# Performance work log

Measured on AMD Instinct MI355X. Metric: run time of the kernel, lower is better.

Reference implementation:

```python
import jax, jax.numpy as jnp
import numpy as np

HID = 1152
NUM_HEADS = 16
NUM_MSK = 2
MLP_HID = int(HID * 4.0)
SCALE = (HID // NUM_HEADS) ** -0.5
EPS = 1e-6


def _ln(t):
    # LayerNorm, elementwise_affine=False, eps=1e-6
    mu = jnp.mean(t, axis=-1, keepdims=True)
    var = jnp.mean(jnp.square(t - mu), axis=-1, keepdims=True)
    return (t - mu) / jnp.sqrt(var + EPS)


def _modulate(t, shift, scale):
    return t * (1.0 + scale[:, None, :]) + shift[:, None, :]


def setup_inputs() -> dict:
    key = jax.random.key(0)
    ks = jax.random.split(key, 12)
    s = 0.02
    return {
        "x": jax.random.normal(ks[0], (8, 4096, HID), jnp.float32),
        "c": jax.random.normal(ks[1], (8, HID), jnp.float32),
        # adaLN_modulation_x: Linear(HID, 6*HID), stored as [in, out]
        "w_ada": jax.random.normal(ks[2], (HID, 6 * HID), jnp.float32) * s,
        "b_ada": jnp.zeros((6 * HID,), jnp.float32),
        # lin1: Linear(HID, 2*HID)
        "w1": jax.random.normal(ks[3], (HID, 2 * HID), jnp.float32) * s,
        "b1": jnp.zeros((2 * HID,), jnp.float32),
        # lin2: Linear(HID, HID)
        "w2": jax.random.normal(ks[4], (HID, HID), jnp.float32) * s,
        "b2": jnp.zeros((HID,), jnp.float32),
        # Mlp: fc1(HID->MLP_HID), gelu(tanh), fc2(MLP_HID->HID)
        "w_fc1": jax.random.normal(ks[5], (HID, MLP_HID), jnp.float32) * s,
        "b_fc1": jnp.zeros((MLP_HID,), jnp.float32),
        "w_fc2": jax.random.normal(ks[6], (MLP_HID, HID), jnp.float32) * s,
        "b_fc2": jnp.zeros((HID,), jnp.float32),
    }


def reference(x, c, w_ada, b_ada, w1, b1, w2, b2, w_fc1, b_fc1, w_fc2, b_fc2):
    B, N, C = x.shape
    # adaLN modulation: SiLU -> Linear, chunk 6 along feature dim
    mods = jax.nn.silu(c) @ w_ada + b_ada  # [B, 6C]
    sh_msa, sc_msa, g_msa, sh_mlp, sc_mlp, g_mlp = jnp.split(mods, 6, axis=1)

    # tiny key/value set from first num_msk tokens
    x0 = x[:, :NUM_MSK, :]  # [B, M, C]
    kv = _modulate(_ln(x0), sh_msa, sc_msa) @ w1 + b1  # [B, M, 2C]
    k, v = jnp.split(kv, 2, axis=2)  # each [B, M, C]
    q = _modulate(_ln(x), sh_msa, sc_msa) @ w2 + b2  # [B, N, C]

    attn = jax.nn.softmax(jnp.einsum("bnc,bmc->bnm", q, k) * SCALE, axis=-1)
    y = jnp.einsum("bnm,bmc->bnc", attn, v)  # [B, N, C]
    # faithful to torch: .transpose(1,2).reshape(B,N,C) (axis scramble, single head)
    y = jnp.swapaxes(y, 1, 2).reshape(B, N, C)
    y = y + g_msa[:, None, :] * y

    h = _modulate(_ln(y), sh_mlp, sc_mlp)
    mlp = jax.nn.gelu(h @ w_fc1 + b_fc1, approximate=True) @ w_fc2 + b_fc2
    return y + g_mlp[:, None, :] * mlp
```

## Files before the change

kernel.cpp:

```cpp
#include <hip/hip_runtime.h>
#include <hip/hip_bf16.h>

#define DEV __device__ __forceinline__

typedef unsigned short u16;
typedef short short8 __attribute__((ext_vector_type(8)));
typedef float f32x4 __attribute__((ext_vector_type(4)));
typedef unsigned long long ulv2 __attribute__((ext_vector_type(2)));

constexpr int HID  = 1152;
constexpr int NSEQ = 4096;
constexpr int NB   = 8;
constexpr int MROWS = NB * NSEQ;
constexpr int MLP  = 4608;
constexpr int NPAD2 = 1280;
constexpr float EPSV  = 1e-6f;
constexpr float SCALE = 0.11785113019775793f;

constexpr size_t O_WT1  = 0;
constexpr size_t SZ_WT1 = (size_t)MLP * HID * 2;
constexpr size_t O_WT2  = O_WT1 + SZ_WT1;
constexpr size_t SZ_WT2 = (size_t)NPAD2 * MLP * 2;
constexpr size_t O_H    = O_WT2 + SZ_WT2;
constexpr size_t SZ_H   = (size_t)MROWS * HID * 2;
constexpr size_t O_MODS = O_H + SZ_H;
constexpr size_t O_K    = O_MODS + (size_t)NB*6912*4;
constexpr size_t O_V    = O_K + (size_t)16*HID*4;
constexpr size_t O_U    = O_V + (size_t)16*HID*4;
constexpr size_t O_A1   = O_U + (size_t)16*HID*4;
constexpr size_t O_S0   = O_A1 + (size_t)16*HID*4;
constexpr size_t O_S1   = O_S0 + 64;
constexpr size_t O_P    = O_S1 + 64;
constexpr size_t O_ACT  = O_P + (size_t)NB*NSEQ*2*4;

#define BARR  asm volatile("s_barrier" ::: "memory")
#define VMW0  asm volatile("s_waitcnt vmcnt(0)" ::: "memory")
#define VMW4  asm volatile("s_waitcnt vmcnt(4)" ::: "memory")
#define VMW8  asm volatile("s_waitcnt vmcnt(8)" ::: "memory")
#define SP1   __builtin_amdgcn_s_setprio(1)
#define SP0   __builtin_amdgcn_s_setprio(0)

DEV u16 f2bf(float f){
  __hip_bfloat16 h = __float2bfloat16(f);
  u16 u; __builtin_memcpy(&u, &h, 2); return u;
}

DEV float wsum(float v){
  #pragma unroll
  for (int o = 32; o; o >>= 1) v += __shfl_xor(v, o, 64);
  return v;
}

DEV void cp16(void* lds, const void* g){
  __builtin_amdgcn_global_load_lds(
      (__attribute__((address_space(1))) void*)g,
      (__attribute__((address_space(3))) void*)lds, 16, 0, 0);
}

__global__ void tcast_k(const float* __restrict__ in, u16* __restrict__ out, int K, int N){
  __shared__ float tile[32][33];
  int n0 = blockIdx.x * 32, k0 = blockIdx.y * 32;
  int tx = threadIdx.x, ty = threadIdx.y;
  #pragma unroll
  for (int i = 0; i < 32; i += 8)
    tile[ty + i][tx] = in[(size_t)(k0 + ty + i) * N + (n0 + tx)];
  __syncthreads();
  #pragma unroll
  for (int i = 0; i < 32; i += 8)
    out[(size_t)(n0 + ty + i) * K + (k0 + tx)] = f2bf(tile[tx][ty + i]);
}

__global__ void mods_k(const float* __restrict__ cv, const float* __restrict__ w_ada,
                       const float* __restrict__ b_ada, float* __restrict__ modsb){
  int b = blockIdx.y;
  __shared__ float cs[HID];
  int tid = threadIdx.x;
  for (int i = tid; i < HID; i += 256){
    float t = cv[b*HID + i];
    cs[i] = t / (1.f + __expf(-t));
  }
  __syncthreads();
  int col = blockIdx.x * 256 + tid;
  float acc = b_ada[col];
  #pragma unroll 4
  for (int k = 0; k < HID; k++) acc += cs[k] * w_ada[(size_t)k*6912 + col];
  modsb[b*6912 + col] = acc;
}

__global__ void kv_k(const float* __restrict__ x, const float* __restrict__ modsb,
                     const float* __restrict__ w1, const float* __restrict__ b1,
                     float* __restrict__ kbuf, float* __restrict__ vbuf){
  int bt = blockIdx.y; int b = bt >> 1, t = bt & 1;
  int tid = threadIdx.x;
  __shared__ float mx[HID];
  __shared__ float rbuf[8];
  __shared__ float s_mu, s_rs;
  const float* xr = x + ((size_t)b*NSEQ + t) * HID;
  float sx = 0.f, sxx = 0.f;
  for (int i = tid; i < HID; i += 256){ float v = xr[i]; sx += v; sxx += v*v; }
  sx = wsum(sx); sxx = wsum(sxx);
  int wave = tid >> 6, lane = tid & 63;
  if (lane == 0){ rbuf[wave] = sx; rbuf[4+wave] = sxx; }
  __syncthreads();
  if (tid == 0){
    float a = rbuf[0]+rbuf[1]+rbuf[2]+rbuf[3];
    float bb = rbuf[4]+rbuf[5]+rbuf[6]+rbuf[7];
    float mu = a * (1.f/HID);
    float var = bb * (1.f/HID) - mu*mu;
    s_mu = mu; s_rs = rsqrtf(var + EPSV);
  }
  __syncthreads();
  float mu = s_mu, rs = s_rs;
  const float* md = modsb + b*6912;
  for (int i = tid; i < HID; i += 256)
    mx[i] = (xr[i]-mu)*rs*(1.f + md[HID+i]) + md[i];
  __syncthreads();
  int col = blockIdx.x * 256 + tid;
  float acc = b1[col];
  #pragma unroll 4
  for (int k = 0; k < HID; k++) acc += mx[k] * w1[(size_t)k*2304 + col];
  if (col < HID) kbuf[bt*HID + col] = acc;
  else           vbuf[bt*HID + col - HID] = acc;
}

__global__ void u2_k(const float* __restrict__ w2, const float* __restrict__ kbuf,
                     const float* __restrict__ modsb, float* __restrict__ ub,
                     float* __restrict__ A1b){
  int bm = blockIdx.y; int b = bm >> 1;
  int tid = threadIdx.x, wave = tid >> 6, lane = tid & 63;
  __shared__ float ks[HID];
  for (int i = tid; i < HID; i += 256) ks[i] = kbuf[bm*HID + i];
  __syncthreads();
  const float* md = modsb + b*6912;
  int j0 = blockIdx.x*16 + wave*4;
  #pragma unroll
  for (int jj = 0; jj < 4; jj++){
    int j = j0 + jj;
    const float* wr = w2 + (size_t)j*HID;
    float acc = 0.f;
    for (int i = lane; i < HID; i += 64) acc += wr[i] * ks[i];
    acc = wsum(acc);
    if (lane == 0){
      ub[bm*HID + j] = acc;
      A1b[bm*HID + j] = (1.f + md[HID + j]) * acc;
    }
  }
}

__global__ void sred_k(const float* __restrict__ ub, const float* __restrict__ A1b,
                       const float* __restrict__ modsb, const float* __restrict__ b2,
                       const float* __restrict__ kbuf, float* __restrict__ S0,
                       float* __restrict__ S1){
  int bm = blockIdx.x; int b = bm >> 1;
  int tid = threadIdx.x;
  float s0 = 0.f, s1 = 0.f;
  const float* md = modsb + b*6912;
  for (int i = tid; i < HID; i += 256){
    s1 += A1b[bm*HID + i];
    s0 += md[i]*ub[bm*HID + i] + b2[i]*kbuf[bm*HID + i];
  }
  s0 = wsum(s0); s1 = wsum(s1);
  __shared__ float rb[16];
  int wave = tid >> 6, lane = tid & 63;
  if (lane == 0){ rb[wave] = s0; rb[8+wave] = s1; }
  __syncthreads();
  if (tid == 0){
    S0[bm] = rb[0]+rb[1]+rb[2]+rb[3];
    S1[bm] = rb[8]+rb[9]+rb[10]+rb[11];
  }
}

__global__ void p_k(const float* __restrict__ x, const float* __restrict__ A1b,
                    const float* __restrict__ S0, const float* __restrict__ S1,
                    float2* __restrict__ pb){
  int tid = threadIdx.x, wave = tid >> 6, lane = tid & 63;
  int row0 = blockIdx.x * 4;
  int b = row0 >> 12;
  __shared__ float a1s[2*HID];
  for (int i = tid; i < 2*HID; i += 256) a1s[i] = A1b[b*2*HID + i];
  __syncthreads();
  int row = row0 + wave;
  const float* xr = x + (size_t)row * HID;
  float sx = 0.f, sxx = 0.f, d0 = 0.f, d1 = 0.f;
  #pragma unroll
  for (int i = 0; i < 9; i++){
    int cc = lane*2 + i*128;
    float2 v = *(const float2*)(xr + cc);
    sx += v.x + v.y; sxx += v.x*v.x + v.y*v.y;
    d0 += v.x*a1s[cc]       + v.y*a1s[cc+1];
    d1 += v.x*a1s[HID+cc]   + v.y*a1s[HID+cc+1];
  }
  sx = wsum(sx); sxx = wsum(sxx); d0 = wsum(d0); d1 = wsum(d1);
  if (lane == 0){
    float mu = sx * (1.f/HID);
    float var = sxx * (1.f/HID) - mu*mu;
    float rs = rsqrtf(var + EPSV);
    float sc0 = rs*(d0 - mu*S1[b*2+0]) + S0[b*2+0];
    float sc1 = rs*(d1 - mu*S1[b*2+1]) + S0[b*2+1];
    float z = (sc0 - sc1) * SCALE;
    float p0 = 1.f / (1.f + __expf(-z));
    pb[row] = make_float2(p0, 1.f - p0);
  }
}

__global__ void h_k(const float2* __restrict__ pb, const float* __restrict__ vbuf,
                    const float* __restrict__ modsb, u16* __restrict__ H){
  int tid = threadIdx.x, wave = tid >> 6, lane = tid & 63;
  int row0 = blockIdx.x * 4;
  int b = row0 >> 12;
  __shared__ float gs[HID], shs[HID], scs[HID];
  const float* md = modsb + b*6912;
  for (int i = tid; i < HID; i += 256){
    gs[i]  = 1.f + md[2*HID + i];
    shs[i] = md[3*HID + i];
    scs[i] = 1.f + md[4*HID + i];
  }
  __syncthreads();
  int row = row0 + wave;
  int n = row & (NSEQ-1);
  const float2* pbb = pb + ((size_t)b << 12);
  const float* vb0 = vbuf + b*2*HID;
  float yv[18];
  float sx = 0.f, sxx = 0.f;
  #pragma unroll
  for (int i = 0; i < 9; i++){
    int cc = lane*2 + i*128;
    int f = n*HID + cc;
    int r0 = f & (NSEQ-1), ci0 = f >> 12;
    int f1 = f + 1;
    int r1 = f1 & (NSEQ-1), ci1 = f1 >> 12;
    float2 pv0 = pbb[r0];
    float2 pv1 = pbb[r1];
    float y0 = gs[cc]   * (pv0.x*vb0[ci0] + pv0.y*vb0[HID+ci0]);
    float y1 = gs[cc+1] * (pv1.x*vb0[ci1] + pv1.y*vb0[HID+ci1]);
    yv[2*i] = y0; yv[2*i+1] = y1;
    sx += y0 + y1; sxx += y0*y0 + y1*y1;
  }
  sx = wsum(sx); sxx = wsum(sxx);
  float mu = sx * (1.f/HID);
  float var = sxx * (1.f/HID) - mu*mu;
  float rs = rsqrtf(var + EPSV);
  u16* Hr = H + (size_t)row * HID;
  #pragma unroll
  for (int i = 0; i < 9; i++){
    int cc = lane*2 + i*128;
    ushort2 st;
    st.x = f2bf((yv[2*i]   - mu)*rs*scs[cc]   + shs[cc]);
    st.y = f2bf((yv[2*i+1] - mu)*rs*scs[cc+1] + shs[cc+1]);
    *(ushort2*)(Hr + cc) = st;
  }
}

template<int EPI, int KC>
__global__ __launch_bounds__(512, 2) void gemm8_k(
    const u16* __restrict__ A, const u16* __restrict__ Bt,
    int nTn,
    const float* __restrict__ bias,
    u16* __restrict__ outB, float* __restrict__ outF,
    const float2* __restrict__ p, const float* __restrict__ vbuf,
    const float* __restrict__ modsb, int rowOffset)
{
  __shared__ u16 lds[2][2][256*64];
  const int tid = threadIdx.x;
  const int wave = tid >> 6, lane = tid & 63;
  const int wm = wave >> 2, wn = wave & 3;

  int nwg = gridDim.x;
  int bid = blockIdx.x;
  int q = nwg >> 3;
  int w = (bid & 7) * q + (bid >> 3);
  int bm = w / nTn, bn = w - bm * nTn;

  const u16* Ab = A + (size_t)bm * 256 * KC;
  const u16* Bb = Bt + (size_t)bn * 256 * KC;

  f32x4 acc[8][4] = {};

  auto stage = [&](int buf, int ab, int half, int t){
    const u16* src = ab ? Bb : Ab;
    char* ldsb = (char*)&lds[buf][ab][0] + half*16384 + wave*2048 + lane*16;
    int rbase = half*128 + wave*16 + (lane>>3);
    int kof = t*64 + (((lane&7) ^ (lane>>3)) << 3);
    cp16(ldsb,        src + (size_t)rbase*KC + kof);
    cp16(ldsb + 1024, src + (size_t)(rbase+8)*KC + kof);
  };
  auto ldA = [&](short8 (&v)[4][2], int buf, int mh){
    const char* base = (const char*)&lds[buf][0][0];
    int colb = (((lane>>4)<<4)) ^ ((lane&7)<<4);
    #pragma unroll
    for (int f = 0; f < 4; f++){
      const char* rp = base + (wm*128 + mh*64 + f*16 + (lane&15))*128;
      v[f][0] = *(const short8*)(rp + colb);
      v[f][1] = *(const short8*)(rp + (colb ^ 64));
    }
  };
  auto ldB = [&](short8 (&v)[2][2], int buf, int nh){
    const char* base = (const char*)&lds[buf][1][0];
    int colb = (((lane>>4)<<4)) ^ ((lane&7)<<4);
    #pragma unroll
    for (int f = 0; f < 2; f++){
      const char* rp = base + (wn*64 + nh*32 + f*16 + (lane&15))*128;
      v[f][0] = *(const short8*)(rp + colb);
      v[f][1] = *(const short8*)(rp + (colb ^ 64));
    }
  };
  auto mm = [&](short8 (&a)[4][2], short8 (&b)[2][2], int mh, int nh){
    #pragma unroll
    for (int ks = 0; ks < 2; ks++)
      #pragma unroll
      for (int f = 0; f < 4; f++)
        #pragma unroll
        for (int g = 0; g < 2; g++)
          acc[mh*4+f][nh*2+g] = __builtin_amdgcn_mfma_f32_16x16x32_bf16(
              a[f][ks], b[g][ks], acc[mh*4+f][nh*2+g], 0, 0, 0);
  };

  short8 av[4][2], av2[4][2], bv[2][2], bv2[2][2];

  stage(0,0,0,0); stage(0,0,1,0); stage(0,1,0,0); stage(0,1,1,0);
  stage(1,1,0,1); stage(1,1,1,1); stage(1,0,0,1); stage(1,0,1,1);
  VMW8; BARR;

  constexpr int NIT = KC >> 7;
  for (int it = 0; it < NIT; ++it){
    const int t2 = 2*it + 2, t3 = 2*it + 3;
    const bool fin = (it == NIT-1);
    ldA(av, 0, 0); ldB(bv, 0, 0);
    SP1; mm(av, bv, 0, 0); SP0; BARR;
    ldB(bv2, 0, 1);
    SP1; mm(av, bv2, 0, 1); SP0; BARR;
    ldA(av2, 0, 1);
    if (!fin) stage(0,1,0,t2);
    SP1; mm(av2, bv, 1, 0); SP0; BARR;
    if (!fin){ stage(0,1,1,t2); VMW4; } else { VMW0; }
    SP1; mm(av2, bv2, 1, 1); SP0; BARR;
    ldA(av, 1, 0); ldB(bv, 1, 0);
    if (!fin){ stage(0,0,0,t2); stage(0,0,1,t2); }
    SP1; mm(av, bv, 0, 0); SP0; BARR;
    ldB(bv2, 1, 1);
    SP1; mm(av, bv2, 0, 1); SP0; BARR;
    ldA(av2, 1, 1);
    if (!fin) stage(1,1,0,t3);
    SP1; mm(av2, bv, 1, 0); SP0; BARR;
    if (!fin){ stage(1,1,1,t3); stage(1,0,0,t3); stage(1,0,1,t3); VMW8; }
    SP1; mm(av2, bv2, 1, 1); SP0; BARR;
  }

  int colBase = bn*256 + wn*64;
  int rowB = bm*256 + wm*128 + ((lane>>4)<<2);
  if constexpr (EPI == 0){
    u16* cs = (u16*)&lds[0][0][0];
    #pragma unroll
    for (int n = 0; n < 4; n++){
      int colL = wn*64 + n*16 + (lane&15);
      float bs = bias[bn*256 + colL];
      #pragma unroll
      for (int m = 0; m < 8; m++){
        #pragma unroll
        for (int r = 0; r < 4; r++){
          int rowL = wm*128 + m*16 + ((lane>>4)<<2) + r;
          float xv = acc[m][n][r] + bs;
          float t = xv * (1.f + 0.044715f * xv * xv);
          float g = xv / (1.f + __expf(-1.5957691216057308f * t));
          int bo = ((rowL*256 + colL)*2) ^ (((rowL>>2)&3)<<5);
          *(u16*)((char*)cs + bo) = f2bf(g);
        }
      }
    }
    __syncthreads();
    #pragma unroll
    for (int e = 0; e < 16; e++){
      int idx = e*512 + tid;
      int rowL = idx >> 5, c16 = idx & 31;
      int bo = (rowL*512 + c16*16) ^ (((rowL>>2)&3)<<5);
      ulv2 v = *(const ulv2*)((const char*)cs + bo);
      __builtin_nontemporal_store(v,
          (ulv2*)&outB[(size_t)(bm*256 + rowL)*MLP + bn*256 + c16*8]);
    }
  } else {
    int bIdx = (rowOffset + bm*256) >> 12;
    const float* md = modsb + bIdx*6912;
    const float2* pbb = p + ((size_t)bIdx << 12);
    const float* vb0 = vbuf + bIdx*2*HID;
    #pragma unroll
    for (int n = 0; n < 4; n++){
      int col = colBase + n*16 + (lane&15);
      if (col < HID){
        float bs = bias[col];
        float gmsa = 1.f + md[2*HID + col];
        float gmlp = md[5*HID + col];
        #pragma unroll
        for (int m = 0; m < 8; m++){
          #pragma unroll
          for (int r = 0; r < 4; r++){
            int grow = rowOffset + rowB + m*16 + r;
            int nn = grow & (NSEQ-1);
            int f = nn*HID + col;
            int rr = f & (NSEQ-1), ci = f >> 12;
            float2 pv = pbb[rr];
            float y2 = gmsa * (pv.x*vb0[ci] + pv.y*vb0[HID + ci]);
            __builtin_nontemporal_store(y2 + gmlp * (acc[m][n][r] + bs),
                &outF[(size_t)grow*HID + col]);
          }
        }
      }
    }
  }
}

extern "C" void kernel_launch(void* const* d_in, const int* in_sizes, int n_in,
                              void* d_out, int out_size, void* d_ws, size_t ws_size,
                              hipStream_t stream){
  const float* x     = (const float*)d_in[0];
  const float* cvec  = (const float*)d_in[1];
  const float* w_ada = (const float*)d_in[2];
  const float* b_ada = (const float*)d_in[3];
  const float* w1    = (const float*)d_in[4];
  const float* b1    = (const float*)d_in[5];
  const float* w2    = (const float*)d_in[6];
  const float* b2    = (const float*)d_in[7];
  const float* w_fc1 = (const float*)d_in[8];
  const float* b_fc1 = (const float*)d_in[9];
  const float* w_fc2 = (const float*)d_in[10];
  const float* b_fc2 = (const float*)d_in[11];
  float* out = (float*)d_out;
  char* ws = (char*)d_ws;

  u16*   Wt1   = (u16*)  (ws + O_WT1);
  u16*   Wt2   = (u16*)  (ws + O_WT2);
  u16*   Hb    = (u16*)  (ws + O_H);
  float* modsb = (float*)(ws + O_MODS);
  float* kb    = (float*)(ws + O_K);
  float* vb    = (float*)(ws + O_V);
  float* ub    = (float*)(ws + O_U);
  float* A1b   = (float*)(ws + O_A1);
  float* S0b   = (float*)(ws + O_S0);
  float* S1b   = (float*)(ws + O_S1);
  float2* pb   = (float2*)(ws + O_P);
  u16*   actb  = (u16*)  (ws + O_ACT);

  (void)hipMemsetAsync(ws + O_WT2 + (size_t)HID*MLP*2, 0, (size_t)(NPAD2-HID)*MLP*2, stream);

  tcast_k<<<dim3(MLP/32, HID/32), dim3(32,8), 0, stream>>>(w_fc1, Wt1, HID, MLP);
  tcast_k<<<dim3(HID/32, MLP/32), dim3(32,8), 0, stream>>>(w_fc2, Wt2, MLP, HID);
  mods_k<<<dim3(27, NB), 256, 0, stream>>>(cvec, w_ada, b_ada, modsb);
  kv_k<<<dim3(9, 16), 256, 0, stream>>>(x, modsb, w1, b1, kb, vb);
  u2_k<<<dim3(HID/16, 16), 256, 0, stream>>>(w2, kb, modsb, ub, A1b);
  sred_k<<<16, 256, 0, stream>>>(ub, A1b, modsb, b2, kb, S0b, S1b);
  p_k<<<MROWS/4, 256, 0, stream>>>(x, A1b, S0b, S1b, pb);
  h_k<<<MROWS/4, 256, 0, stream>>>(pb, vb, modsb, Hb);

  size_t actFull = (size_t)MROWS * MLP * 2;
  int nch = 1;
  while (nch < 8 && O_ACT + actFull/nch > ws_size) nch <<= 1;
  int rowsPer = MROWS / nch;

  for (int chn = 0; chn < nch; chn++){
    int r0 = chn * rowsPer;
    int nTm = rowsPer / 256;
    gemm8_k<0, HID><<<nTm*(MLP/256), 512, 0, stream>>>(
        Hb + (size_t)r0*HID, Wt1, MLP/256, b_fc1,
        actb, nullptr, nullptr, nullptr, nullptr, 0);
    gemm8_k<1, MLP><<<nTm*(NPAD2/256), 512, 0, stream>>>(
        actb, Wt2, NPAD2/256, b_fc2,
        nullptr, out, pb, vb, modsb, r0);
  }
  (void)in_sizes; (void)n_in; (void)out_size;
}
```

Baseline: 1.120 ms.

## Make GEMMs persistent and prefetch next tile during epilogue

Both MLP GEMMs now launch a fixed 256-workgroup persistent grid that loops over output tiles. The first K-slab of the next tile is prefetched into LDS during the last iteration, and the second slab is issued after the epilogue. The intent is to hide the pipeline fill and epilogue latency between tiles. The epilogues are restaged through the other LDS buffer in row passes, and the fc2 output now goes out as coalesced 16-byte stores instead of scattered scalar stores. This adds extra barriers, and the hand-counted vmcnt waits (24/40) must match the outstanding loads exactly.

Result: slower. 2.105 ms (+88.0%).

```diff
diff --git a/kernel.cpp b/kernel.cpp
--- a/kernel.cpp
+++ b/kernel.cpp
@@ -33,10 +33,12 @@
 constexpr size_t O_P    = O_S1 + 64;
 constexpr size_t O_ACT  = O_P + (size_t)NB*NSEQ*2*4;
 
-#define BARR  asm volatile("s_barrier" ::: "memory")
-#define VMW0  asm volatile("s_waitcnt vmcnt(0)" ::: "memory")
-#define VMW4  asm volatile("s_waitcnt vmcnt(4)" ::: "memory")
-#define VMW8  asm volatile("s_waitcnt vmcnt(8)" ::: "memory")
+#define BARR   asm volatile("s_barrier" ::: "memory")
+#define VMW0   asm volatile("s_waitcnt vmcnt(0)" ::: "memory")
+#define VMW4   asm volatile("s_waitcnt vmcnt(4)" ::: "memory")
+#define VMW8   asm volatile("s_waitcnt vmcnt(8)" ::: "memory")
+#define VMW24  asm volatile("s_waitcnt vmcnt(24)" ::: "memory")
+#define VMW40  asm volatile("s_waitcnt vmcnt(40)" ::: "memory")
 #define SP1   __builtin_amdgcn_s_setprio(1)
 #define SP0   __builtin_amdgcn_s_setprio(0)
 
@@ -252,9 +254,9 @@
 }
 
 template<int EPI, int KC>
-__global__ __launch_bounds__(512, 2) void gemm8_k(
+__global__ __launch_bounds__(512, 2) void gemmp_k(
     const u16* __restrict__ A, const u16* __restrict__ Bt,
-    int nTn,
+    int nTiles, int nTn,
     const float* __restrict__ bias,
     u16* __restrict__ outB, float* __restrict__ outF,
     const float2* __restrict__ p, const float* __restrict__ vbuf,
@@ -264,29 +266,22 @@
   const int tid = threadIdx.x;
   const int wave = tid >> 6, lane = tid & 63;
   const int wm = wave >> 2, wn = wave & 3;
-
-  int nwg = gridDim.x;
-  int bid = blockIdx.x;
-  int q = nwg >> 3;
-  int w = (bid & 7) * q + (bid >> 3);
-  int bm = w / nTn, bn = w - bm * nTn;
-
-  const u16* Ab = A + (size_t)bm * 256 * KC;
-  const u16* Bb = Bt + (size_t)bn * 256 * KC;
-
-  f32x4 acc[8][4] = {};
-
-  auto stage = [&](int buf, int ab, int half, int t){
-    const u16* src = ab ? Bb : Ab;
+  const int q = nTiles >> 3;
+
+  auto swz = [&](int bid, int& bm, int& bn){
+    int w = (bid & 7) * q + (bid >> 3);
+    bm = w / nTn; bn = w - bm * nTn;
+  };
+  auto stageTo = [&](int buf, int ab, int half, const u16* src, int tof){
     char* ldsb = (char*)&lds[buf][ab][0] + half*16384 + wave*2048 + lane*16;
     int rbase = half*128 + wave*16 + (lane>>3);
-    int kof = t*64 + (((lane&7) ^ (lane>>3)) << 3);
+    int kof = tof + (((lane&7) ^ (lane>>3)) << 3);
     cp16(ldsb,        src + (size_t)rbase*KC + kof);
     cp16(ldsb + 1024, src + (size_t)(rbase+8)*KC + kof);
   };
+  const int colb = (((lane>>4)<<4)) ^ ((lane&7)<<4);
   auto ldA = [&](short8 (&v)[4][2], int buf, int mh){
     const char* base = (const char*)&lds[buf][0][0];
-    int colb = (((lane>>4)<<4)) ^ ((lane&7)<<4);
     #pragma unroll
     for (int f = 0; f < 4; f++){
       const char* rp = base + (wm*128 + mh*64 + f*16 + (lane&15))*128;
@@ -296,7 +291,6 @@
   };
   auto ldB = [&](short8 (&v)[2][2], int buf, int nh){
     const char* base = (const char*)&lds[buf][1][0];
-    int colb = (((lane>>4)<<4)) ^ ((lane&7)<<4);
     #pragma unroll
     for (int f = 0; f < 2; f++){
       const char* rp = base + (wn*64 + nh*32 + f*16 + (lane&15))*128;
@@ -304,106 +298,163 @@
       v[f][1] = *(const short8*)(rp + (colb ^ 64));
     }
   };
-  auto mm = [&](short8 (&a)[4][2], short8 (&b)[2][2], int mh, int nh){
-    #pragma unroll
-    for (int ks = 0; ks < 2; ks++)
+
+  for (int tt = 0;; ++tt){
+    int bid = tid*0 + blockIdx.x + (int)gridDim.x * tt;
+    if (bid >= nTiles) break;
+    int bm, bn; swz(bid, bm, bn);
+    const u16* Ab = A + (size_t)bm * 256 * KC;
+    const u16* Bb = Bt + (size_t)bn * 256 * KC;
+    int bidN = bid + (int)gridDim.x;
+    const bool hasNext = bidN < nTiles;
+    int bmN = bm, bnN = bn;
+    if (hasNext) swz(bidN, bmN, bnN);
+    const u16* AbN = A + (size_t)bmN * 256 * KC;
+    const u16* BbN = Bt + (size_t)bnN * 256 * KC;
+
+    if (tt == 0){
+      stageTo(0,0,0,Ab,0);  stageTo(0,0,1,Ab,0);  stageTo(0,1,0,Bb,0);  stageTo(0,1,1,Bb,0);
+      stageTo(1,1,0,Bb,64); stageTo(1,1,1,Bb,64); stageTo(1,0,0,Ab,64); stageTo(1,0,1,Ab,64);
+      VMW8;
+    } else {
+      if constexpr (EPI == 0) { VMW24; } else { VMW40; }
+    }
+    BARR;
+
+    f32x4 acc[8][4] = {};
+    short8 av[4][2], av2[4][2], bv[2][2], bv2[2][2];
+    auto mm = [&](short8 (&a)[4][2], short8 (&b)[2][2], int mh, int nh){
       #pragma unroll
-      for (int f = 0; f < 4; f++)
+      for (int ks = 0; ks < 2; ks++)
         #pragma unroll
-        for (int g = 0; g < 2; g++)
-          acc[mh*4+f][nh*2+g] = __builtin_amdgcn_mfma_f32_16x16x32_bf16(
-              a[f][ks], b[g][ks], acc[mh*4+f][nh*2+g], 0, 0, 0);
-  };
-
-  short8 av[4][2], av2[4][2], bv[2][2], bv2[2][2];
-
-  stage(0,0,0,0); stage(0,0,1,0); stage(0,1,0,0); stage(0,1,1,0);
-  stage(1,1,0,1); stage(1,1,1,1); stage(1,0,0,1); stage(1,0,1,1);
-  VMW8; BARR;
-
-  constexpr int NIT = KC >> 7;
-  for (int it = 0; it < NIT; ++it){
-    const int t2 = 2*it + 2, t3 = 2*it + 3;
-    const bool fin = (it == NIT-1);
-    ldA(av, 0, 0); ldB(bv, 0, 0);
-    SP1; mm(av, bv, 0, 0); SP0; BARR;
-    ldB(bv2, 0, 1);
-    SP1; mm(av, bv2, 0, 1); SP0; BARR;
-    ldA(av2, 0, 1);
-    if (!fin) stage(0,1,0,t2);
-    SP1; mm(av2, bv, 1, 0); SP0; BARR;
-    if (!fin){ stage(0,1,1,t2); VMW4; } else { VMW0; }
-    SP1; mm(av2, bv2, 1, 1); SP0; BARR;
-    ldA(av, 1, 0); ldB(bv, 1, 0);
-    if (!fin){ stage(0,0,0,t2); stage(0,0,1,t2); }
-    SP1; mm(av, bv, 0, 0); SP0; BARR;
-    ldB(bv2, 1, 1);
-    SP1; mm(av, bv2, 0, 1); SP0; BARR;
-    ldA(av2, 1, 1);
-    if (!fin) stage(1,1,0,t3);
-    SP1; mm(av2, bv, 1, 0); SP0; BARR;
-    if (!fin){ stage(1,1,1,t3); stage(1,0,0,t3); stage(1,0,1,t3); VMW8; }
-    SP1; mm(av2, bv2, 1, 1); SP0; BARR;
-  }
-
-  int colBase = bn*256 + wn*64;
-  int rowB = bm*256 + wm*128 + ((lane>>4)<<2);
-  if constexpr (EPI == 0){
-    u16* cs = (u16*)&lds[0][0][0];
-    #pragma unroll
-    for (int n = 0; n < 4; n++){
-      int colL = wn*64 + n*16 + (lane&15);
-      float bs = bias[bn*256 + colL];
+        for (int f = 0; f < 4; f++)
+          #pragma unroll
+          for (int g = 0; g < 2; g++)
+            acc[mh*4+f][nh*2+g] = __builtin_amdgcn_mfma_f32_16x16x32_bf16(
+                a[f][ks], b[g][ks], acc[mh*4+f][nh*2+g], 0, 0, 0);
+    };
+
+    constexpr int NIT = KC >> 7;
+    for (int it = 0; it < NIT; ++it){
+      const bool fin = (it == NIT-1);
+      const u16* As2 = fin ? AbN : Ab;
+      const u16* Bs2 = fin ? BbN : Bb;
+      const int t2o = fin ? 0 : (2*it+2)*64;
+      const int t3o = (2*it+3)*64;
+      const bool do2 = !fin || hasNext;
+      ldA(av, 0, 0); ldB(bv, 0, 0);
+      SP1; mm(av, bv, 0, 0); SP0; BARR;
+      ldB(bv2, 0, 1);
+      SP1; mm(av, bv2, 0, 1); SP0; BARR;
+      ldA(av2, 0, 1);
+      if (do2) stageTo(0,1,0,Bs2,t2o);
+      SP1; mm(av2, bv, 1, 0); SP0; BARR;
+      if (do2){ stageTo(0,1,1,Bs2,t2o); VMW4; } else { VMW0; }
+      SP1; mm(av2, bv2, 1, 1); SP0; BARR;
+      ldA(av, 1, 0); ldB(bv, 1, 0);
+      if (do2){ stageTo(0,0,0,As2,t2o); stageTo(0,0,1,As2,t2o); }
+      SP1; mm(av, bv, 0, 0); SP0; BARR;
+      ldB(bv2, 1, 1);
+      SP1; mm(av, bv2, 0, 1); SP0; BARR;
+      ldA(av2, 1, 1);
+      if (!fin) stageTo(1,1,0,Bb,t3o);
+      SP1; mm(av2, bv, 1, 0); SP0; BARR;
+      if (!fin){ stageTo(1,1,1,Bb,t3o); stageTo(1,0,0,Ab,t3o); stageTo(1,0,1,Ab,t3o); VMW8; }
+      SP1; mm(av2, bv2, 1, 1); SP0; BARR;
+    }
+
+    if constexpr (EPI == 0){
+      u16* cs = (u16*)&lds[1][0][0];
       #pragma unroll
-      for (int m = 0; m < 8; m++){
-        #pragma unroll
-        for (int r = 0; r < 4; r++){
-          int rowL = wm*128 + m*16 + ((lane>>4)<<2) + r;
-          float xv = acc[m][n][r] + bs;
-          float t = xv * (1.f + 0.044715f * xv * xv);
-          float g = xv / (1.f + __expf(-1.5957691216057308f * t));
-          int bo = ((rowL*256 + colL)*2) ^ (((rowL>>2)&3)<<5);
-          *(u16*)((char*)cs + bo) = f2bf(g);
-        }
-      }
-    }
-    __syncthreads();
-    #pragma unroll
-    for (int e = 0; e < 16; e++){
-      int idx = e*512 + tid;
-      int rowL = idx >> 5, c16 = idx & 31;
-      int bo = (rowL*512 + c16*16) ^ (((rowL>>2)&3)<<5);
-      ulv2 v = *(const ulv2*)((const char*)cs + bo);
-      __builtin_nontemporal_store(v,
-          (ulv2*)&outB[(size_t)(bm*256 + rowL)*MLP + bn*256 + c16*8]);
-    }
-  } else {
-    int bIdx = (rowOffset + bm*256) >> 12;
-    const float* md = modsb + bIdx*6912;
-    const float2* pbb = p + ((size_t)bIdx << 12);
-    const float* vb0 = vbuf + bIdx*2*HID;
-    #pragma unroll
-    for (int n = 0; n < 4; n++){
-      int col = colBase + n*16 + (lane&15);
-      if (col < HID){
-        float bs = bias[col];
-        float gmsa = 1.f + md[2*HID + col];
-        float gmlp = md[5*HID + col];
-        #pragma unroll
-        for (int m = 0; m < 8; m++){
+      for (int pass = 0; pass < 2; ++pass){
+        if (wm == pass){
           #pragma unroll
-          for (int r = 0; r < 4; r++){
-            int grow = rowOffset + rowB + m*16 + r;
-            int nn = grow & (NSEQ-1);
-            int f = nn*HID + col;
-            int rr = f & (NSEQ-1), ci = f >> 12;
-            float2 pv = pbb[rr];
-            float y2 = gmsa * (pv.x*vb0[ci] + pv.y*vb0[HID + ci]);
-            __builtin_nontemporal_store(y2 + gmlp * (acc[m][n][r] + bs),
-                &outF[(size_t)grow*HID + col]);
+          for (int n = 0; n < 4; n++){
+            int colL = wn*64 + n*16 + (lane&15);
+            float bs = bias[bn*256 + colL];
+            #pragma unroll
+            for (int m = 0; m < 8; m++){
+              #pragma unroll
+              for (int r = 0; r < 4; r++){
+                int rowS = m*16 + ((lane>>4)<<2) + r;
+                float xv = acc[m][n][r] + bs;
+                float t = xv * (1.f + 0.044715f * xv * xv);
+                float g = xv / (1.f + __expf(-1.5957691216057308f * t));
+                int bo = ((rowS*256 + colL)*2) ^ (((rowS>>2)&3)<<5);
+                *(u16*)((char*)cs + bo) = f2bf(g);
+              }
+            }
           }
         }
+        __syncthreads();
+        #pragma unroll
+        for (int e = 0; e < 8; e++){
+          int idx = e*512 + tid;
+          int rowS = idx >> 5, c16 = idx & 31;
+          int bo = (rowS*512 + c16*16) ^ (((rowS>>2)&3)<<5);
+          ulv2 v = *(const ulv2*)((const char*)cs + bo);
+          __builtin_nontemporal_store(v,
+              (ulv2*)&outB[(size_t)(bm*256 + pass*128 + rowS)*MLP + bn*256 + c16*8]);
+        }
+        __syncthreads();
       }
+    } else {
+      float* cf = (float*)&lds[1][0][0];
+      int bIdx = (rowOffset + bm*256) >> 12;
+      const float* md = modsb + bIdx*6912;
+      const float2* pbb = p + ((size_t)bIdx << 12);
+      const float* vb0 = vbuf + bIdx*2*HID;
+      #pragma unroll
+      for (int pass = 0; pass < 4; ++pass){
+        if (wm == (pass>>1)){
+          int mb = (pass&1)*4;
+          #pragma unroll
+          for (int n = 0; n < 4; n++){
+            int colL = wn*64 + n*16 + (lane&15);
+            int col = bn*256 + colL;
+            float bs = 0.f, gmsa = 0.f, gmlp = 0.f;
+            if (col < HID){ bs = bias[col]; gmsa = 1.f + md[2*HID+col]; gmlp = md[5*HID+col]; }
+            #pragma unroll
+            for (int mi = 0; mi < 4; mi++){
+              #pragma unroll
+              for (int r = 0; r < 4; r++){
+                int rowS = mi*16 + ((lane>>4)<<2) + r;
+                float val = 0.f;
+                if (col < HID){
+                  int grow = rowOffset + bm*256 + pass*64 + rowS;
+                  int nn = grow & (NSEQ-1);
+                  int f = nn*HID + col;
+                  int rr = f & (NSEQ-1), ci = f >> 12;
+                  float2 pv = pbb[rr];
+                  float y2 = gmsa * (pv.x*vb0[ci] + pv.y*vb0[HID + ci]);
+                  val = y2 + gmlp * (acc[mb+mi][n][r] + bs);
+                }
+                int bo = ((rowS*256 + colL)*4) ^ (((rowS>>2)&3)<<5);
+                *(float*)((char*)cf + bo) = val;
+              }
+            }
+          }
+        }
+        __syncthreads();
+        #pragma unroll
+        for (int e = 0; e < 8; e++){
+          int idx = e*512 + tid;
+          int rowS = idx >> 6, s4 = idx & 63;
+          int col0 = bn*256 + s4*4;
+          if (col0 < HID){
+            int bo = (rowS*1024 + s4*16) ^ (((rowS>>2)&3)<<5);
+            f32x4 v = *(const f32x4*)((const char*)cf + bo);
+            __builtin_nontemporal_store(v,
+                (f32x4*)&outF[(size_t)(rowOffset + bm*256 + pass*64 + rowS)*HID + col0]);
+          }
+        }
+        __syncthreads();
+      }
+    }
+
+    if (hasNext){
+      stageTo(1,1,0,BbN,64); stageTo(1,1,1,BbN,64);
+      stageTo(1,0,0,AbN,64); stageTo(1,0,1,AbN,64);
     }
   }
 }
@@ -458,11 +509,11 @@
   for (int chn = 0; chn < nch; chn++){
     int r0 = chn * rowsPer;
     int nTm = rowsPer / 256;
-    gemm8_k<0, HID><<<nTm*(MLP/256), 512, 0, stream>>>(
-        Hb + (size_t)r0*HID, Wt1, MLP/256, b_fc1,
+    gemmp_k<0, HID><<<256, 512, 0, stream>>>(
+        Hb + (size_t)r0*HID, Wt1, nTm*(MLP/256), MLP/256, b_fc1,
         actb, nullptr, nullptr, nullptr, nullptr, 0);
-    gemm8_k<1, MLP><<<nTm*(NPAD2/256), 512, 0, stream>>>(
-        actb, Wt2, NPAD2/256, b_fc2,
+    gemmp_k<1, MLP><<<256, 512, 0, stream>>>(
+        actb, Wt2, nTm*(NPAD2/256), NPAD2/256, b_fc2,
         nullptr, out, pb, vb, modsb, r0);
   }
   (void)in_sizes; (void)n_in; (void)out_size;
```
